# Kernel tuning notes

Measured on AMD Instinct MI355X. Metric: run time of the kernel, lower is better.

The kernel has to match this reference:

```python
import jax, jax.numpy as jnp
import numpy as np

N = 100000        # number of nodes
E = 1600000       # number of edges (avg degree 16)
D_IN = 512
D_OUT = 64


def setup_inputs() -> dict:
    key = jax.random.key(0)
    k1, k2, k3, k4, k5 = jax.random.split(key, 5)
    inputs = jax.random.normal(k1, (N, D_IN), dtype=jnp.float32)
    weight = jax.random.normal(k2, (D_IN, D_OUT), dtype=jnp.float32)
    adj_vals = jax.random.uniform(k3, (E,), dtype=jnp.float32)
    adj_rows = jax.random.randint(k4, (E,), 0, N, dtype=jnp.int32)
    adj_cols = jax.random.randint(k5, (E,), 0, N, dtype=jnp.int32)
    return {
        "inputs": inputs,
        "weight": weight,
        "adj_vals": adj_vals,
        "adj_rows": adj_rows,
        "adj_cols": adj_cols,
    }


def reference(inputs, weight, adj_vals, adj_rows, adj_cols):
    # Dense projection: [N, D_IN] @ [D_IN, D_OUT] -> [N, D_OUT]
    h = inputs @ weight
    # Sparse adjacency spmm (COO): out[r] += vals[e] * h[c] for edge e=(r,c)
    msgs = adj_vals[:, None] * h[adj_cols]            # [E, D_OUT]
    agg = jax.ops.segment_sum(msgs, adj_rows, num_segments=N)  # [N, D_OUT]
    # activation = relu
    return jax.nn.relu(agg)
```

## Files before the change

### kernel.cpp

```cpp
#include <hip/hip_runtime.h>
#include <hip/hip_bf16.h>

#define D_OUT 64
#define K_DIM 512
#define RPB 128
#define RPB_SHIFT 7
#define EPB 8192
#define GCAP 3072
#define RCAP 3072
#define CPAD 16
#define NBK 1024

using short8  = __attribute__((ext_vector_type(8))) short;
using floatx4 = __attribute__((ext_vector_type(4))) float;

__device__ inline unsigned short f32_to_bf16(float f) {
    __hip_bfloat16 b = __float2bfloat16(f);
    return *reinterpret_cast<unsigned short*>(&b);
}

__device__ inline unsigned int pk_bf16(float lo, float hi) {
    __hip_bfloat162 p = __float22bfloat162_rn(make_float2(lo, hi));
    return *reinterpret_cast<unsigned int*>(&p);
}

__device__ inline float bf16lo_f32(unsigned int g) {
    return __uint_as_float(g << 16);
}
__device__ inline float bf16hi_f32(unsigned int g) {
    return __uint_as_float(g & 0xFFFF0000u);
}

__global__ void wt_kernel(const float* __restrict__ W, unsigned short* __restrict__ wt,
                          int* __restrict__ cursor, int nbuck) {
    int i = blockIdx.x * blockDim.x + threadIdx.x;
    if (i < D_OUT * K_DIM) {
        int n = i >> 9;
        int k = i & 511;
        wt[i] = f32_to_bf16(W[k * D_OUT + n]);
    }
    if (i < nbuck) cursor[i * CPAD] = i * GCAP;
}

__global__ __launch_bounds__(256) void gemm_part_kernel(
    const float* __restrict__ A, const unsigned short* __restrict__ wt,
    unsigned short* __restrict__ H, int n,
    const int* __restrict__ rows, const int* __restrict__ cols,
    const float* __restrict__ vals, int* __restrict__ cursor,
    int2* __restrict__ keys, int E, int nbuck, int npart) {
    __shared__ int sm[2 * NBK];

    const int tid = threadIdx.x;

    if (blockIdx.x < npart) {
        int* cnt  = sm;
        int* offs = sm + NBK;
        const int blk = blockIdx.x;

        for (int b = tid; b < nbuck; b += 256) cnt[b] = 0;
        __syncthreads();

        const int base = blk * EPB;
#pragma unroll
        for (int i = 0; i < EPB / 256; i++) {
            int e = base + tid + i * 256;
            if (e < E) atomicAdd(&cnt[rows[e] >> RPB_SHIFT], 1);
        }
        __syncthreads();

        for (int b = tid; b < nbuck; b += 256) {
            int c = cnt[b];
            offs[b] = c ? atomicAdd(&cursor[b * CPAD], c) : 0;
        }
        __syncthreads();

#pragma unroll
        for (int i = 0; i < EPB / 256; i++) {
            int e = base + tid + i * 256;
            if (e < E) {
                int r = rows[e];
                int c = cols[e];
                float v = vals[e];
                int b = r >> RPB_SHIFT;
                int p = atomicAdd(&offs[b], 1);
                if (p < (b + 1) * GCAP)
                    keys[p] = make_int2(c | ((r & (RPB - 1)) << 17), __float_as_int(v));
            }
        }
        return;
    }

    const int gb   = blockIdx.x - npart;
    const int wv   = tid >> 6;
    const int lane = tid & 63;
    const int ln   = lane & 15;
    const int quad = lane >> 4;
    const int row0 = gb * 64 + wv * 16;

    int arow = row0 + ln;
    if (arow >= n) arow = n - 1;
    const float* Arow = A + (size_t)arow * K_DIM;
    const unsigned short* wb = wt + (size_t)ln * K_DIM;

    floatx4 acc0 = {0.f, 0.f, 0.f, 0.f};
    floatx4 acc1 = {0.f, 0.f, 0.f, 0.f};
    floatx4 acc2 = {0.f, 0.f, 0.f, 0.f};
    floatx4 acc3 = {0.f, 0.f, 0.f, 0.f};

    for (int h0 = 0; h0 < K_DIM; h0 += 128) {
        float4 t[8];
#pragma unroll
        for (int s = 0; s < 4; s++) {
            t[2 * s]     = *reinterpret_cast<const float4*>(Arow + h0 + s * 32 + quad * 8);
            t[2 * s + 1] = *reinterpret_cast<const float4*>(Arow + h0 + s * 32 + quad * 8 + 4);
        }
        short8 ab[4];
#pragma unroll
        for (int s = 0; s < 4; s++) {
            float4 a0 = t[2 * s], a1 = t[2 * s + 1];
            int4 pk;
            pk.x = (int)pk_bf16(a0.x, a0.y);
            pk.y = (int)pk_bf16(a0.z, a0.w);
            pk.z = (int)pk_bf16(a1.x, a1.y);
            pk.w = (int)pk_bf16(a1.z, a1.w);
            ab[s] = *reinterpret_cast<short8*>(&pk);
        }
#pragma unroll
        for (int s = 0; s < 4; s++) {
            const int ko = h0 + s * 32 + quad * 8;
            short8 b0 = *reinterpret_cast<const short8*>(wb + ko);
            short8 b1 = *reinterpret_cast<const short8*>(wb + 16 * K_DIM + ko);
            short8 b2 = *reinterpret_cast<const short8*>(wb + 32 * K_DIM + ko);
            short8 b3 = *reinterpret_cast<const short8*>(wb + 48 * K_DIM + ko);
            acc0 = __builtin_amdgcn_mfma_f32_16x16x32_bf16(ab[s], b0, acc0, 0, 0, 0);
            acc1 = __builtin_amdgcn_mfma_f32_16x16x32_bf16(ab[s], b1, acc1, 0, 0, 0);
            acc2 = __builtin_amdgcn_mfma_f32_16x16x32_bf16(ab[s], b2, acc2, 0, 0, 0);
            acc3 = __builtin_amdgcn_mfma_f32_16x16x32_bf16(ab[s], b3, acc3, 0, 0, 0);
        }
    }

#pragma unroll
    for (int r = 0; r < 4; r++) {
        int gr = row0 + quad * 4 + r;
        if (gr < n) {
            unsigned short* Hr = H + (size_t)gr * D_OUT;
            Hr[ln]      = f32_to_bf16(acc0[r]);
            Hr[16 + ln] = f32_to_bf16(acc1[r]);
            Hr[32 + ln] = f32_to_bf16(acc2[r]);
            Hr[48 + ln] = f32_to_bf16(acc3[r]);
        }
    }
}

__global__ __launch_bounds__(512) void sort_agg_kernel(
    const unsigned short* __restrict__ h, const int2* __restrict__ keys,
    const int* __restrict__ cursor, float* __restrict__ out, int N) {
    __shared__ int2 rec[RCAP];
    __shared__ int cnt[RPB];
    __shared__ int excl[RPB];
    __shared__ int cur[RPB];
    __shared__ int wtot[2];

    const int tid  = threadIdx.x;
    const int lane = tid & 63;
    const int wv   = tid >> 6;
    const int q    = lane >> 4;
    const int li   = lane & 15;
    const int b    = blockIdx.x;

    const int start = b * GCAP;
    int m = cursor[b * CPAD] - start;
    if (m > GCAP) m = GCAP;

    if (tid < RPB) cnt[tid] = 0;
    __syncthreads();

    for (int i = tid; i < m; i += 512) {
        int rl = keys[start + i].x >> 17;
        atomicAdd(&cnt[rl], 1);
    }
    __syncthreads();

    int v = 0, x = 0;
    if (tid < RPB) {
        v = cnt[tid];
        x = v;
#pragma unroll
        for (int d = 1; d < 64; d <<= 1) {
            int y = __shfl_up(x, d, 64);
            if (lane >= d) x += y;
        }
        if (lane == 63) wtot[tid >> 6] = x;
    }
    __syncthreads();
    if (tid < RPB) {
        int base = (tid >= 64) ? wtot[0] : 0;
        int ex = base + x - v;
        excl[tid] = ex;
        cur[tid]  = ex;
    }
    __syncthreads();

    for (int i = tid; i < m; i += 512) {
        int2 kv = keys[start + i];
        int rl = kv.x >> 17;
        int p = atomicAdd(&cur[rl], 1);
        if (p < RCAP) rec[p] = kv;
    }
    __syncthreads();

    const int row0 = b * RPB;
    for (int rl = wv; rl < RPB; rl += 8) {
        int s = excl[rl];
        int e = cur[rl];
        float4 acc = {0.f, 0.f, 0.f, 0.f};
        int j = s;
        for (; j + 8 <= e; j += 8) {
            int2 kA = rec[j + q];
            int2 kB = rec[j + 4 + q];
            const uint2 gA = *reinterpret_cast<const uint2*>(
                h + (size_t)(kA.x & 0x1FFFF) * D_OUT + li * 4);
            const uint2 gB = *reinterpret_cast<const uint2*>(
                h + (size_t)(kB.x & 0x1FFFF) * D_OUT + li * 4);
            float vA = __int_as_float(kA.y);
            float vB = __int_as_float(kB.y);
            acc.x += vA * bf16lo_f32(gA.x);
            acc.y += vA * bf16hi_f32(gA.x);
            acc.z += vA * bf16lo_f32(gA.y);
            acc.w += vA * bf16hi_f32(gA.y);
            acc.x += vB * bf16lo_f32(gB.x);
            acc.y += vB * bf16hi_f32(gB.x);
            acc.z += vB * bf16lo_f32(gB.y);
            acc.w += vB * bf16hi_f32(gB.y);
        }
        for (; j < e; j += 4) {
            bool on = (j + q) < e;
            int2 kv = rec[on ? j + q : j];
            const uint2 g = *reinterpret_cast<const uint2*>(
                h + (size_t)(kv.x & 0x1FFFF) * D_OUT + li * 4);
            float vv = on ? __int_as_float(kv.y) : 0.f;
            acc.x += vv * bf16lo_f32(g.x);
            acc.y += vv * bf16hi_f32(g.x);
            acc.z += vv * bf16lo_f32(g.y);
            acc.w += vv * bf16hi_f32(g.y);
        }
        acc.x += __shfl_xor(acc.x, 16, 64);
        acc.y += __shfl_xor(acc.y, 16, 64);
        acc.z += __shfl_xor(acc.z, 16, 64);
        acc.w += __shfl_xor(acc.w, 16, 64);
        acc.x += __shfl_xor(acc.x, 32, 64);
        acc.y += __shfl_xor(acc.y, 32, 64);
        acc.z += __shfl_xor(acc.z, 32, 64);
        acc.w += __shfl_xor(acc.w, 32, 64);

        if (q == 0) {
            int gr = row0 + rl;
            if (gr < N) {
                float4 o;
                o.x = fmaxf(acc.x, 0.f);
                o.y = fmaxf(acc.y, 0.f);
                o.z = fmaxf(acc.z, 0.f);
                o.w = fmaxf(acc.w, 0.f);
                *reinterpret_cast<float4*>(out + (size_t)gr * D_OUT + li * 4) = o;
            }
        }
    }
}

extern "C" void kernel_launch(void* const* d_in, const int* in_sizes, int n_in,
                              void* d_out, int out_size, void* d_ws, size_t ws_size,
                              hipStream_t stream) {
    const float* A    = (const float*)d_in[0];
    const float* W    = (const float*)d_in[1];
    const float* vals = (const float*)d_in[2];
    const int*   rows = (const int*)d_in[3];
    const int*   cols = (const int*)d_in[4];
    float* out = (float*)d_out;

    const int N = out_size / D_OUT;
    const int E = in_sizes[2];
    const int nbuck = (N + RPB - 1) >> RPB_SHIFT;
    const int nb = (E + EPB - 1) / EPB;
    const int gb = (N + 63) / 64;

    char* ws = (char*)d_ws;
    unsigned short* h      = (unsigned short*)ws;
    int2*           keys   = (int2*)(ws + (size_t)N * D_OUT * 2);
    unsigned short* wt     = (unsigned short*)((char*)keys + (size_t)nbuck * GCAP * 8);
    int*            cursor = (int*)((char*)wt + (size_t)D_OUT * K_DIM * 2);

    wt_kernel<<<(D_OUT * K_DIM + 255) / 256, 256, 0, stream>>>(W, wt, cursor, nbuck);
    gemm_part_kernel<<<nb + gb, 256, 0, stream>>>(A, wt, h, N,
                                                  rows, cols, vals, cursor, keys,
                                                  E, nbuck, nb);
    sort_agg_kernel<<<nbuck, 512, 0, stream>>>(h, keys, cursor, out, N);
}
```

Baseline: 384.3 us.

## Pre-swizzle bf16 weights into MFMA fragment order and compute two row tiles per wave

The weight transpose kernel now writes bf16 weights in the exact per-lane MFMA B-fragment order, so each lane's B loads become contiguous, coalesced 16-byte reads. Each GEMM wave now computes two 16-row tiles (128 rows per block), reusing every loaded B fragment across both tiles. This halves weight traffic per output row and the GEMM block count. The cost is about twice the accumulator and A-staging registers, which may lower occupancy for the memory-bound streaming of the input matrix.

```diff
diff --git a/kernel.cpp b/kernel.cpp
--- a/kernel.cpp
+++ b/kernel.cpp
@@ -31,19 +31,23 @@
     return __uint_as_float(g & 0xFFFF0000u);
 }
 
-__global__ void wt_kernel(const float* __restrict__ W, unsigned short* __restrict__ wt,
+__global__ void wt_kernel(const float* __restrict__ W, unsigned short* __restrict__ wf,
                           int* __restrict__ cursor, int nbuck) {
     int i = blockIdx.x * blockDim.x + threadIdx.x;
     if (i < D_OUT * K_DIM) {
-        int n = i >> 9;
-        int k = i & 511;
-        wt[i] = f32_to_bf16(W[k * D_OUT + n]);
+        int j    = i & 7;
+        int lane = (i >> 3) & 63;
+        int s    = (i >> 9) & 15;
+        int nb   = i >> 13;
+        int k  = s * 32 + (lane >> 4) * 8 + j;
+        int nn = nb * 16 + (lane & 15);
+        wf[i] = f32_to_bf16(W[k * D_OUT + nn]);
     }
     if (i < nbuck) cursor[i * CPAD] = i * GCAP;
 }
 
 __global__ __launch_bounds__(256) void gemm_part_kernel(
-    const float* __restrict__ A, const unsigned short* __restrict__ wt,
+    const float* __restrict__ A, const unsigned short* __restrict__ wf,
     unsigned short* __restrict__ H, int n,
     const int* __restrict__ rows, const int* __restrict__ cols,
     const float* __restrict__ vals, int* __restrict__ cursor,
@@ -90,52 +94,67 @@
         return;
     }
 
-    const int gb   = blockIdx.x - npart;
+    const int gbk  = blockIdx.x - npart;
     const int wv   = tid >> 6;
     const int lane = tid & 63;
     const int ln   = lane & 15;
     const int quad = lane >> 4;
-    const int row0 = gb * 64 + wv * 16;
-
-    int arow = row0 + ln;
-    if (arow >= n) arow = n - 1;
-    const float* Arow = A + (size_t)arow * K_DIM;
-    const unsigned short* wb = wt + (size_t)ln * K_DIM;
-
-    floatx4 acc0 = {0.f, 0.f, 0.f, 0.f};
-    floatx4 acc1 = {0.f, 0.f, 0.f, 0.f};
-    floatx4 acc2 = {0.f, 0.f, 0.f, 0.f};
-    floatx4 acc3 = {0.f, 0.f, 0.f, 0.f};
+    const int row0 = gbk * 128 + wv * 16;
+    const int row1 = row0 + 64;
+
+    int a0 = row0 + ln; if (a0 >= n) a0 = n - 1;
+    int a1 = row1 + ln; if (a1 >= n) a1 = n - 1;
+    const float* Arow0 = A + (size_t)a0 * K_DIM;
+    const float* Arow1 = A + (size_t)a1 * K_DIM;
+    const unsigned short* wfl = wf + lane * 8;
+
+    floatx4 accA0 = {0.f,0.f,0.f,0.f}, accA1 = {0.f,0.f,0.f,0.f};
+    floatx4 accA2 = {0.f,0.f,0.f,0.f}, accA3 = {0.f,0.f,0.f,0.f};
+    floatx4 accB0 = {0.f,0.f,0.f,0.f}, accB1 = {0.f,0.f,0.f,0.f};
+    floatx4 accB2 = {0.f,0.f,0.f,0.f}, accB3 = {0.f,0.f,0.f,0.f};
 
     for (int h0 = 0; h0 < K_DIM; h0 += 128) {
-        float4 t[8];
+        float4 t0[8], t1[8];
 #pragma unroll
         for (int s = 0; s < 4; s++) {
-            t[2 * s]     = *reinterpret_cast<const float4*>(Arow + h0 + s * 32 + quad * 8);
-            t[2 * s + 1] = *reinterpret_cast<const float4*>(Arow + h0 + s * 32 + quad * 8 + 4);
-        }
-        short8 ab[4];
+            t0[2 * s]     = *reinterpret_cast<const float4*>(Arow0 + h0 + s * 32 + quad * 8);
+            t0[2 * s + 1] = *reinterpret_cast<const float4*>(Arow0 + h0 + s * 32 + quad * 8 + 4);
+            t1[2 * s]     = *reinterpret_cast<const float4*>(Arow1 + h0 + s * 32 + quad * 8);
+            t1[2 * s + 1] = *reinterpret_cast<const float4*>(Arow1 + h0 + s * 32 + quad * 8 + 4);
+        }
+        short8 ab0[4], ab1[4];
 #pragma unroll
         for (int s = 0; s < 4; s++) {
-            float4 a0 = t[2 * s], a1 = t[2 * s + 1];
+            float4 x0 = t0[2 * s], x1 = t0[2 * s + 1];
             int4 pk;
-            pk.x = (int)pk_bf16(a0.x, a0.y);
-            pk.y = (int)pk_bf16(a0.z, a0.w);
-            pk.z = (int)pk_bf16(a1.x, a1.y);
-            pk.w = (int)pk_bf16(a1.z, a1.w);
-            ab[s] = *reinterpret_cast<short8*>(&pk);
+            pk.x = (int)pk_bf16(x0.x, x0.y);
+            pk.y = (int)pk_bf16(x0.z, x0.w);
+            pk.z = (int)pk_bf16(x1.x, x1.y);
+            pk.w = (int)pk_bf16(x1.z, x1.w);
+            ab0[s] = *reinterpret_cast<short8*>(&pk);
+            float4 y0 = t1[2 * s], y1 = t1[2 * s + 1];
+            int4 qk;
+            qk.x = (int)pk_bf16(y0.x, y0.y);
+            qk.y = (int)pk_bf16(y0.z, y0.w);
+            qk.z = (int)pk_bf16(y1.x, y1.y);
+            qk.w = (int)pk_bf16(y1.z, y1.w);
+            ab1[s] = *reinterpret_cast<short8*>(&qk);
         }
 #pragma unroll
         for (int s = 0; s < 4; s++) {
-            const int ko = h0 + s * 32 + quad * 8;
-            short8 b0 = *reinterpret_cast<const short8*>(wb + ko);
-            short8 b1 = *reinterpret_cast<const short8*>(wb + 16 * K_DIM + ko);
-            short8 b2 = *reinterpret_cast<const short8*>(wb + 32 * K_DIM + ko);
-            short8 b3 = *reinterpret_cast<const short8*>(wb + 48 * K_DIM + ko);
-            acc0 = __builtin_amdgcn_mfma_f32_16x16x32_bf16(ab[s], b0, acc0, 0, 0, 0);
-            acc1 = __builtin_amdgcn_mfma_f32_16x16x32_bf16(ab[s], b1, acc1, 0, 0, 0);
-            acc2 = __builtin_amdgcn_mfma_f32_16x16x32_bf16(ab[s], b2, acc2, 0, 0, 0);
-            acc3 = __builtin_amdgcn_mfma_f32_16x16x32_bf16(ab[s], b3, acc3, 0, 0, 0);
+            const unsigned short* base = wfl + h0 * 16 + s * 512;
+            short8 b0 = *reinterpret_cast<const short8*>(base);
+            short8 b1 = *reinterpret_cast<const short8*>(base + 8192);
+            short8 b2 = *reinterpret_cast<const short8*>(base + 16384);
+            short8 b3 = *reinterpret_cast<const short8*>(base + 24576);
+            accA0 = __builtin_amdgcn_mfma_f32_16x16x32_bf16(ab0[s], b0, accA0, 0, 0, 0);
+            accA1 = __builtin_amdgcn_mfma_f32_16x16x32_bf16(ab0[s], b1, accA1, 0, 0, 0);
+            accA2 = __builtin_amdgcn_mfma_f32_16x16x32_bf16(ab0[s], b2, accA2, 0, 0, 0);
+            accA3 = __builtin_amdgcn_mfma_f32_16x16x32_bf16(ab0[s], b3, accA3, 0, 0, 0);
+            accB0 = __builtin_amdgcn_mfma_f32_16x16x32_bf16(ab1[s], b0, accB0, 0, 0, 0);
+            accB1 = __builtin_amdgcn_mfma_f32_16x16x32_bf16(ab1[s], b1, accB1, 0, 0, 0);
+            accB2 = __builtin_amdgcn_mfma_f32_16x16x32_bf16(ab1[s], b2, accB2, 0, 0, 0);
+            accB3 = __builtin_amdgcn_mfma_f32_16x16x32_bf16(ab1[s], b3, accB3, 0, 0, 0);
         }
     }
 
@@ -144,10 +163,21 @@
         int gr = row0 + quad * 4 + r;
         if (gr < n) {
             unsigned short* Hr = H + (size_t)gr * D_OUT;
-            Hr[ln]      = f32_to_bf16(acc0[r]);
-            Hr[16 + ln] = f32_to_bf16(acc1[r]);
-            Hr[32 + ln] = f32_to_bf16(acc2[r]);
-            Hr[48 + ln] = f32_to_bf16(acc3[r]);
+            Hr[ln]      = f32_to_bf16(accA0[r]);
+            Hr[16 + ln] = f32_to_bf16(accA1[r]);
+            Hr[32 + ln] = f32_to_bf16(accA2[r]);
+            Hr[48 + ln] = f32_to_bf16(accA3[r]);
+        }
+    }
+#pragma unroll
+    for (int r = 0; r < 4; r++) {
+        int gr = row1 + quad * 4 + r;
+        if (gr < n) {
+            unsigned short* Hr = H + (size_t)gr * D_OUT;
+            Hr[ln]      = f32_to_bf16(accB0[r]);
+            Hr[16 + ln] = f32_to_bf16(accB1[r]);
+            Hr[32 + ln] = f32_to_bf16(accB2[r]);
+            Hr[48 + ln] = f32_to_bf16(accB3[r]);
         }
     }
 }
@@ -281,16 +311,16 @@
     const int E = in_sizes[2];
     const int nbuck = (N + RPB - 1) >> RPB_SHIFT;
     const int nb = (E + EPB - 1) / EPB;
-    const int gb = (N + 63) / 64;
+    const int gb = (N + 127) / 128;
 
     char* ws = (char*)d_ws;
     unsigned short* h      = (unsigned short*)ws;
     int2*           keys   = (int2*)(ws + (size_t)N * D_OUT * 2);
-    unsigned short* wt     = (unsigned short*)((char*)keys + (size_t)nbuck * GCAP * 8);
-    int*            cursor = (int*)((char*)wt + (size_t)D_OUT * K_DIM * 2);
-
-    wt_kernel<<<(D_OUT * K_DIM + 255) / 256, 256, 0, stream>>>(W, wt, cursor, nbuck);
-    gemm_part_kernel<<<nb + gb, 256, 0, stream>>>(A, wt, h, N,
+    unsigned short* wf     = (unsigned short*)((char*)keys + (size_t)nbuck * GCAP * 8);
+    int*            cursor = (int*)((char*)wf + (size_t)D_OUT * K_DIM * 2);
+
+    wt_kernel<<<(D_OUT * K_DIM + 255) / 256, 256, 0, stream>>>(W, wf, cursor, nbuck);
+    gemm_part_kernel<<<nb + gb, 256, 0, stream>>>(A, wf, h, N,
                                                   rows, cols, vals, cursor, keys,
                                                   E, nbuck, nb);
     sort_agg_kernel<<<nbuck, 512, 0, stream>>>(h, keys, cursor, out, N);
```

After: 384.2 us. Within noise of the previous version (-0.0%).
